# Performance work log

Measured on AMD Instinct MI355X. Metric: run time of the kernel, lower is better.

## Reference

```python
import jax, jax.numpy as jnp
import numpy as np

B, S, D, H, DK, F, K = 8, 1024, 512, 8, 64, 2048, 31
EPS = 1e-5


def _ln(x, g, b):
    m = jnp.mean(x, -1, keepdims=True)
    v = jnp.mean((x - m) ** 2, -1, keepdims=True)
    return (x - m) * jax.lax.rsqrt(v + EPS) * g + b


def _ff(x, w1, b1, w2, b2):
    return jnp.maximum(x @ w1 + b1, 0.0) @ w2 + b2


def setup_inputs() -> dict:
    key = jax.random.key(0)
    ks = jax.random.split(key, 16)
    w = lambda k, shape: jax.random.normal(k, shape, dtype=jnp.float32) * 0.02
    inp = {"x": jax.random.normal(ks[0], (B, S, D), dtype=jnp.float32)}
    for name in ["norm1", "norm2", "norm3", "norm4", "conv_ln"]:
        inp[name + "_g"] = jnp.ones((D,), jnp.float32)
        inp[name + "_b"] = jnp.zeros((D,), jnp.float32)
    # feed-forward 1 and 2
    inp["ff1_w1"] = w(ks[1], (D, F)); inp["ff1_b1"] = jnp.zeros((F,), jnp.float32)
    inp["ff1_w2"] = w(ks[2], (F, D)); inp["ff1_b2"] = jnp.zeros((D,), jnp.float32)
    inp["ff2_w1"] = w(ks[3], (D, F)); inp["ff2_b1"] = jnp.zeros((F,), jnp.float32)
    inp["ff2_w2"] = w(ks[4], (F, D)); inp["ff2_b2"] = jnp.zeros((D,), jnp.float32)
    # attention projections ([in, out] layout)
    inp["wq"] = w(ks[5], (D, D)); inp["bq"] = jnp.zeros((D,), jnp.float32)
    inp["wk"] = w(ks[6], (D, D)); inp["bk"] = jnp.zeros((D,), jnp.float32)
    inp["wv"] = w(ks[7], (D, D)); inp["bv"] = jnp.zeros((D,), jnp.float32)
    inp["wo"] = w(ks[8], (D, D)); inp["bo"] = jnp.zeros((D,), jnp.float32)
    # convolution module
    inp["pw1_w"] = w(ks[9], (D, 2 * D)); inp["pw1_b"] = jnp.zeros((2 * D,), jnp.float32)
    inp["dw_w"] = w(ks[10], (D, 1, K)); inp["dw_b"] = jnp.zeros((D,), jnp.float32)
    inp["bn_g"] = jnp.ones((D,), jnp.float32); inp["bn_b"] = jnp.zeros((D,), jnp.float32)
    inp["bn_mean"] = jnp.zeros((D,), jnp.float32); inp["bn_var"] = jnp.ones((D,), jnp.float32)
    inp["pw2_w"] = w(ks[11], (D, D)); inp["pw2_b"] = jnp.zeros((D,), jnp.float32)
    return inp


def _forward(x, norm1_g, norm1_b, norm2_g, norm2_b, norm3_g, norm3_b, norm4_g, norm4_b,
             ff1_w1, ff1_b1, ff1_w2, ff1_b2, wq, bq, wk, bk, wv, bv, wo, bo,
             conv_ln_g, conv_ln_b, pw1_w, pw1_b, dw_w, dw_b,
             bn_g, bn_b, bn_mean, bn_var, pw2_w, pw2_b,
             ff2_w1, ff2_b1, ff2_w2, ff2_b2):
    b, s, _ = x.shape
    # half-step FF1
    x = x + 0.5 * _ff(_ln(x, norm1_g, norm1_b), ff1_w1, ff1_b1, ff1_w2, ff1_b2)
    # multi-head self-attention (pre-norm)
    h = _ln(x, norm2_g, norm2_b)
    q = (h @ wq + bq).reshape(b, s, H, DK)
    k = (h @ wk + bk).reshape(b, s, H, DK)
    v = (h @ wv + bv).reshape(b, s, H, DK)
    scores = jnp.einsum("bqhd,bkhd->bhqk", q, k) / jnp.sqrt(jnp.asarray(DK, x.dtype))
    attn = jax.nn.softmax(scores, axis=-1)
    o = jnp.einsum("bhqk,bkhd->bqhd", attn, v).reshape(b, s, D)
    x = x + (o @ wo + bo)
    # convolution module (pre-norm)
    h = _ln(x, norm3_g, norm3_b)
    h = _ln(h, conv_ln_g, conv_ln_b)
    h = h @ pw1_w + pw1_b                                 # [B,S,2D] pointwise conv1
    h = h[..., :D] * jax.nn.sigmoid(h[..., D:])           # GLU over channels
    h = h.transpose(0, 2, 1)                              # [B,D,S]
    h = jax.lax.conv_general_dilated(
        h, dw_w, window_strides=(1,), padding=((K // 2, K // 2),),
        feature_group_count=D, dimension_numbers=("NCH", "OIH", "NCH")) + dw_b[:, None]
    h = (h - bn_mean[:, None]) * jax.lax.rsqrt(bn_var + EPS)[:, None] * bn_g[:, None] + bn_b[:, None]
    h = h * jax.nn.sigmoid(h)                             # SiLU
    h = jnp.einsum("bcl,co->bol", h, pw2_w) + pw2_b[:, None]
    x = x + h.transpose(0, 2, 1)
    # half-step FF2
    x = x + 0.5 * _ff(_ln(x, norm4_g, norm4_b), ff2_w1, ff2_b1, ff2_w2, ff2_b2)
    return x


def reference(x, norm1_g, norm1_b, norm2_g, norm2_b, norm3_g, norm3_b, norm4_g, norm4_b,
              conv_ln_g, conv_ln_b, ff1_w1, ff1_b1, ff1_w2, ff1_b2,
              ff2_w1, ff2_b1, ff2_w2, ff2_b2, wq, bq, wk, bk, wv, bv, wo, bo,
              pw1_w, pw1_b, dw_w, dw_b, bn_g, bn_b, bn_mean, bn_var, pw2_w, pw2_b):
    return _forward(x, norm1_g, norm1_b, norm2_g, norm2_b, norm3_g, norm3_b, norm4_g, norm4_b,
                    ff1_w1, ff1_b1, ff1_w2, ff1_b2, wq, bq, wk, bk, wv, bv, wo, bo,
                    conv_ln_g, conv_ln_b, pw1_w, pw1_b, dw_w, dw_b,
                    bn_g, bn_b, bn_mean, bn_var, pw2_w, pw2_b,
                    ff2_w1, ff2_b1, ff2_w2, ff2_b2)
```

## Files before the change

### kernel.cpp

```cpp
#include <hip/hip_runtime.h>
#include <math.h>

#define TOK    8192
#define DMODEL 512
#define FDIM   2048
#define NH     8
#define DKH    64
#define SEQ    1024
#define BATCH  8
#define KCONV  31
#define LN_EPS 1e-5f

typedef __attribute__((ext_vector_type(8))) short bf16x8;
typedef __attribute__((ext_vector_type(4))) float f32x4;
typedef unsigned short ushort_t;

#define AS1 __attribute__((address_space(1)))
#define AS3 __attribute__((address_space(3)))

__device__ __forceinline__ float sigf(float x) { return 1.0f / (1.0f + __expf(-x)); }

__device__ __forceinline__ unsigned short f2bf(float f) {
  unsigned u = __float_as_uint(f);
  u = u + 0x7fffu + ((u >> 16) & 1u);
  return (unsigned short)(u >> 16);
}
__device__ __forceinline__ unsigned pk2(float a, float b) {
  return (unsigned)f2bf(a) | ((unsigned)f2bf(b) << 16);
}
__device__ __forceinline__ float bf2f(ushort_t u) {
  return __uint_as_float((unsigned)u << 16);
}

__device__ __forceinline__ void xcd_swizzle(int gx, int* bx, int* by) {
  const int nwg = gx * (int)gridDim.y;
  const int cpx = nwg >> 3;
  const int bid = (*by) * gx + (*bx);
  const int wg = (bid & 7) * cpx + (bid >> 3);
  *bx = wg % gx;
  *by = wg / gx;
}

struct WJob { const float* src; ushort_t* dst; int K, N, t0; };
struct WJobs {
  WJob j[10];
  int misc_t0;
  const float* dww; const float* bq; const float* bk; const float* bv;
  float* wTc; float* bcat;
};

__global__ __launch_bounds__(256) void wcast_all(WJobs jobs) {
  __shared__ float tile[32][33];
  const int t = blockIdx.x;
  const int tx = threadIdx.x, ty = threadIdx.y;
  if (t >= jobs.misc_t0) {
    const int idx = (t - jobs.misc_t0) * 256 + ty * 32 + tx;
    if (idx < DMODEL * KCONV) {
      const int d = idx / KCONV, k = idx % KCONV;
      jobs.wTc[k * DMODEL + d] = jobs.dww[idx];
    } else if (idx < DMODEL * KCONV + 3 * DMODEL) {
      const int c = idx - DMODEL * KCONV;
      jobs.bcat[c] = (c < DMODEL) ? jobs.bq[c]
                    : (c < 2 * DMODEL ? jobs.bk[c - DMODEL] : jobs.bv[c - 2 * DMODEL]);
    }
    return;
  }
  int i = 0;
#pragma unroll
  for (int k = 1; k < 10; ++k) if (t >= jobs.j[k].t0) i = k;
  const WJob jb = jobs.j[i];
  const int local = t - jb.t0;
  const int ntx = jb.N >> 5;
  const int bx = (local % ntx) * 32, by = (local / ntx) * 32;
#pragma unroll
  for (int r = 0; r < 32; r += 8)
    tile[ty + r][tx] = jb.src[(size_t)(by + ty + r) * jb.N + bx + tx];
  __syncthreads();
#pragma unroll
  for (int r = 0; r < 32; r += 8)
    jb.dst[(size_t)(bx + ty + r) * jb.K + by + tx] = f2bf(tile[tx][ty + r]);
}

template <bool OBF>
__global__ __launch_bounds__(256) void ln_kernel(const float* __restrict__ in,
                                                 const float* __restrict__ g,
                                                 const float* __restrict__ b,
                                                 void* __restrict__ outp) {
  const int wave = threadIdx.x >> 6, lane = threadIdx.x & 63;
  const size_t row = (size_t)blockIdx.x * 4 + wave;
  const float* p = in + row * DMODEL + lane * 8;
  const float4 v0 = *(const float4*)p;
  const float4 v1 = *(const float4*)(p + 4);
  float s  = v0.x + v0.y + v0.z + v0.w + v1.x + v1.y + v1.z + v1.w;
  float ss = v0.x*v0.x + v0.y*v0.y + v0.z*v0.z + v0.w*v0.w
           + v1.x*v1.x + v1.y*v1.y + v1.z*v1.z + v1.w*v1.w;
#pragma unroll
  for (int m = 1; m < 64; m <<= 1) { s += __shfl_xor(s, m); ss += __shfl_xor(ss, m); }
  const float mean = s * (1.0f / DMODEL);
  const float var  = ss * (1.0f / DMODEL) - mean * mean;
  const float rstd = rsqrtf(var + LN_EPS);
  const float4 g0 = *(const float4*)(g + lane * 8);
  const float4 g1 = *(const float4*)(g + lane * 8 + 4);
  const float4 bb0 = *(const float4*)(b + lane * 8);
  const float4 bb1 = *(const float4*)(b + lane * 8 + 4);
  float o[8];
  o[0] = (v0.x - mean) * rstd * g0.x + bb0.x;
  o[1] = (v0.y - mean) * rstd * g0.y + bb0.y;
  o[2] = (v0.z - mean) * rstd * g0.z + bb0.z;
  o[3] = (v0.w - mean) * rstd * g0.w + bb0.w;
  o[4] = (v1.x - mean) * rstd * g1.x + bb1.x;
  o[5] = (v1.y - mean) * rstd * g1.y + bb1.y;
  o[6] = (v1.z - mean) * rstd * g1.z + bb1.z;
  o[7] = (v1.w - mean) * rstd * g1.w + bb1.w;
  if (OBF) {
    uint4 pkv;
    pkv.x = pk2(o[0], o[1]); pkv.y = pk2(o[2], o[3]);
    pkv.z = pk2(o[4], o[5]); pkv.w = pk2(o[6], o[7]);
    *(uint4*)((ushort_t*)outp + row * DMODEL + lane * 8) = pkv;
  } else {
    float4 a, c;
    a.x = o[0]; a.y = o[1]; a.z = o[2]; a.w = o[3];
    c.x = o[4]; c.y = o[5]; c.z = o[6]; c.w = o[7];
    float* q = (float*)outp + row * DMODEL + lane * 8;
    *(float4*)q = a;
    *(float4*)(q + 4) = c;
  }
}

__global__ __launch_bounds__(256) void ln2_kernel(const float* __restrict__ in,
                                                  const float* __restrict__ g1,
                                                  const float* __restrict__ b1,
                                                  const float* __restrict__ g2,
                                                  const float* __restrict__ b2,
                                                  ushort_t* __restrict__ outp) {
  const int wave = threadIdx.x >> 6, lane = threadIdx.x & 63;
  const size_t row = (size_t)blockIdx.x * 4 + wave;
  const float* p = in + row * DMODEL + lane * 8;
  float v[8];
  {
    const float4 v0 = *(const float4*)p;
    const float4 v1 = *(const float4*)(p + 4);
    v[0]=v0.x; v[1]=v0.y; v[2]=v0.z; v[3]=v0.w;
    v[4]=v1.x; v[5]=v1.y; v[6]=v1.z; v[7]=v1.w;
  }
  float s = 0.f, ss = 0.f;
#pragma unroll
  for (int e = 0; e < 8; ++e) { s += v[e]; ss += v[e]*v[e]; }
#pragma unroll
  for (int m = 1; m < 64; m <<= 1) { s += __shfl_xor(s, m); ss += __shfl_xor(ss, m); }
  float mean = s * (1.0f / DMODEL);
  float rstd = rsqrtf(ss * (1.0f / DMODEL) - mean * mean + LN_EPS);
  const float4 ga = *(const float4*)(g1 + lane * 8);
  const float4 gb = *(const float4*)(g1 + lane * 8 + 4);
  const float4 ba = *(const float4*)(b1 + lane * 8);
  const float4 bb = *(const float4*)(b1 + lane * 8 + 4);
  const float gg1[8] = {ga.x,ga.y,ga.z,ga.w,gb.x,gb.y,gb.z,gb.w};
  const float bb1[8] = {ba.x,ba.y,ba.z,ba.w,bb.x,bb.y,bb.z,bb.w};
#pragma unroll
  for (int e = 0; e < 8; ++e) v[e] = (v[e] - mean) * rstd * gg1[e] + bb1[e];
  s = 0.f; ss = 0.f;
#pragma unroll
  for (int e = 0; e < 8; ++e) { s += v[e]; ss += v[e]*v[e]; }
#pragma unroll
  for (int m = 1; m < 64; m <<= 1) { s += __shfl_xor(s, m); ss += __shfl_xor(ss, m); }
  mean = s * (1.0f / DMODEL);
  rstd = rsqrtf(ss * (1.0f / DMODEL) - mean * mean + LN_EPS);
  const float4 gc = *(const float4*)(g2 + lane * 8);
  const float4 gd = *(const float4*)(g2 + lane * 8 + 4);
  const float4 bc = *(const float4*)(b2 + lane * 8);
  const float4 bd = *(const float4*)(b2 + lane * 8 + 4);
  const float gg2[8] = {gc.x,gc.y,gc.z,gc.w,gd.x,gd.y,gd.z,gd.w};
  const float bb2[8] = {bc.x,bc.y,bc.z,bc.w,bd.x,bd.y,bd.z,bd.w};
  float o[8];
#pragma unroll
  for (int e = 0; e < 8; ++e) o[e] = (v[e] - mean) * rstd * gg2[e] + bb2[e];
  uint4 pkv;
  pkv.x = pk2(o[0], o[1]); pkv.y = pk2(o[2], o[3]);
  pkv.z = pk2(o[4], o[5]); pkv.w = pk2(o[6], o[7]);
  *(uint4*)(outp + row * DMODEL + lane * 8) = pkv;
}

template <int ACT, bool QSC>
__global__ __launch_bounds__(512, 2) void gemm256(const ushort_t* __restrict__ A,
                                                  const ushort_t* __restrict__ Bt,
                                                  const float* __restrict__ bias,
                                                  ushort_t* __restrict__ Cout,
                                                  int N) {
  __shared__ ushort_t lds[65536];
  const int t = threadIdx.x;
  const int l = t & 63;
  const int wid = t >> 6;
  const int wm = wid >> 2, wn = wid & 3;
  int bx = blockIdx.x, by = blockIdx.y;
  xcd_swizzle(gridDim.x, &bx, &by);
  const int m0 = by * 256, n0 = bx * 256;
  const int K = 512;

  f32x4 acc[8][4];
#pragma unroll
  for (int m = 0; m < 8; ++m)
#pragma unroll
    for (int n = 0; n < 4; ++n) acc[m][n] = (f32x4){0.f, 0.f, 0.f, 0.f};

  const int srow = t >> 3;
  const int schunk = (t & 7) ^ ((t >> 3) & 7);

#define STAGE_A(TAU, C_, I_)                                                    \
  __builtin_amdgcn_global_load_lds(                                             \
      (const AS1 unsigned*)(A + (size_t)(m0 + (I_) * 64 + srow) * K +           \
                            (TAU) * 64 + schunk * 8),                           \
      (AS3 unsigned*)(lds + (C_) * 16384 + ((I_) * 512 + t) * 8), 16, 0, 0)
#define STAGE_B(TAU, C_, I_)                                                    \
  __builtin_amdgcn_global_load_lds(                                             \
      (const AS1 unsigned*)(Bt + (size_t)(n0 + (I_) * 64 + srow) * K +          \
                            (TAU) * 64 + schunk * 8),                           \
      (AS3 unsigned*)(lds + 32768 + (C_) * 16384 + ((I_) * 512 + t) * 8), 16, 0, 0)

#pragma unroll
  for (int i = 0; i < 4; ++i) STAGE_B(0, 0, i);
#pragma unroll
  for (int i = 0; i < 4; ++i) STAGE_A(0, 0, i);
#pragma unroll
  for (int i = 0; i < 4; ++i) STAGE_B(1, 1, i);
  STAGE_A(1, 1, 0);
  STAGE_A(1, 1, 2);
  asm volatile("s_waitcnt vmcnt(6)" ::: "memory");
  __builtin_amdgcn_s_barrier();

  const int arow = (l & 15);
  const int kch0 = (l >> 4);
  bf16x8 bfr[2][4];

  for (int it = 0; it < 4; ++it) {
    const bool stg = (it < 3);
#pragma unroll
    for (int h = 0; h < 2; ++h) {
      const int c = h;
#pragma unroll
      for (int p = 0; p < 4; ++p) {
        bf16x8 afr[2][2];
#pragma unroll
        for (int m2 = 0; m2 < 2; ++m2)
#pragma unroll
          for (int ks = 0; ks < 2; ++ks) {
            const int row = wm * 128 + (2 * p + m2) * 16 + arow;
            const int ch = (ks * 4 + kch0) ^ (row & 7);
            afr[m2][ks] = *(const bf16x8*)(lds + c * 16384 + row * 64 + ch * 8);
          }
        if (p == 0) {
#pragma unroll
          for (int nr = 0; nr < 4; ++nr)
#pragma unroll
            for (int ks = 0; ks < 2; ++ks) {
              const int row = wn * 64 + nr * 16 + arow;
              const int ch = (ks * 4 + kch0) ^ (row & 7);
              bfr[ks][nr] = *(const bf16x8*)(lds + 32768 + c * 16384 + row * 64 + ch * 8);
            }
        }
        if (p == 0) {
          if (h == 0 || stg) {
            STAGE_A(2 * it + h + 1, c ^ 1, 1);
            STAGE_A(2 * it + h + 1, c ^ 1, 3);
          }
        } else if (p == 1) {
          if (stg) {
#pragma unroll
            for (int i = 0; i < 4; ++i) STAGE_B(2 * it + h + 2, c, i);
          }
        } else if (p == 2) {
          if (stg) {
            STAGE_A(2 * it + h + 2, c, 0);
            STAGE_A(2 * it + h + 2, c, 2);
          }
        }
        __builtin_amdgcn_s_barrier();
        __builtin_amdgcn_s_setprio(1);
#pragma unroll
        for (int ks = 0; ks < 2; ++ks)
#pragma unroll
          for (int m2 = 0; m2 < 2; ++m2)
#pragma unroll
            for (int nr = 0; nr < 4; ++nr)
              acc[2 * p + m2][nr] = __builtin_amdgcn_mfma_f32_16x16x32_bf16(
                  afr[m2][ks], bfr[ks][nr], acc[2 * p + m2][nr], 0, 0, 0);
        __builtin_amdgcn_s_setprio(0);
        if (p == 3) {
          if (h == 0) {
            if (stg) asm volatile("s_waitcnt vmcnt(6)" ::: "memory");
            else     asm volatile("s_waitcnt vmcnt(0)" ::: "memory");
          } else if (stg) {
            asm volatile("s_waitcnt vmcnt(6)" ::: "memory");
          }
        }
        __builtin_amdgcn_s_barrier();
      }
    }
  }
#undef STAGE_A
#undef STAGE_B

#pragma unroll
  for (int m = 0; m < 8; ++m) {
    const int row_b = m0 + wm * 128 + m * 16 + (l >> 4) * 4;
#pragma unroll
    for (int n = 0; n < 4; ++n) {
      const int col = n0 + wn * 64 + n * 16 + (l & 15);
      const float bv = bias[col];
      const float sc = QSC ? (col < DMODEL ? 0.125f : 1.0f) : 1.0f;
#pragma unroll
      for (int j = 0; j < 4; ++j) {
        float v = acc[m][n][j] + bv;
        if (ACT == 1) v = fmaxf(v, 0.f);
        v *= sc;
        Cout[(size_t)(row_b + j) * N + col] = f2bf(v);
      }
    }
  }
}

template <int TN, int ACT, bool RES, bool OBF, bool QSC>
__global__ __launch_bounds__(256) void gemm_bf16(const ushort_t* __restrict__ A,
                                                 const ushort_t* __restrict__ Bt,
                                                 const float* __restrict__ bias,
                                                 const float* __restrict__ Rp,
                                                 float alpha,
                                                 void* __restrict__ Cout,
                                                 int M, int N, int K) {
  constexpr int NF = TN / 32;
  constexpr int NB = TN / 32;
  __shared__ ushort_t Al[128 * 64];
  __shared__ ushort_t Bl[TN * 64];
  const int t = threadIdx.x;
  const int lane = t & 63;
  const int wid = t >> 6;
  const int wr = wid >> 1, wc = wid & 1;
  int bx = blockIdx.x, by = blockIdx.y;
  xcd_swizzle(gridDim.x, &bx, &by);
  const int m0 = by * 128, n0 = bx * TN;

  f32x4 acc[4][NF];
#pragma unroll
  for (int m = 0; m < 4; ++m)
#pragma unroll
    for (int n = 0; n < NF; ++n) acc[m][n] = (f32x4){0.f, 0.f, 0.f, 0.f};

  const int srow = t >> 3;
  const int scol = (t & 7) * 8;
  const ushort_t* Ag = A + (size_t)(m0 + srow) * K + scol;
  const ushort_t* Bg = Bt + (size_t)(n0 + srow) * K + scol;

  for (int k0 = 0; k0 < K; k0 += 64) {
    __syncthreads();
#pragma unroll
    for (int i = 0; i < 4; ++i) {
      __builtin_amdgcn_global_load_lds(
          (const AS1 unsigned*)(Ag + (size_t)i * 32 * K + k0),
          (AS3 unsigned*)(Al + ((size_t)i * 256 + t) * 8),
          16, 0, 0);
    }
#pragma unroll
    for (int i = 0; i < NB; ++i) {
      __builtin_amdgcn_global_load_lds(
          (const AS1 unsigned*)(Bg + (size_t)i * 32 * K + k0),
          (AS3 unsigned*)(Bl + ((size_t)i * 256 + t) * 8),
          16, 0, 0);
    }
    __syncthreads();

#pragma unroll
    for (int ks = 0; ks < 2; ++ks) {
      const int kk = ks * 32 + (lane >> 4) * 8;
      bf16x8 af[4], bfv[NF];
#pragma unroll
      for (int m = 0; m < 4; ++m)
        af[m] = *(const bf16x8*)(Al + (wr * 64 + m * 16 + (lane & 15)) * 64 + kk);
#pragma unroll
      for (int n = 0; n < NF; ++n)
        bfv[n] = *(const bf16x8*)(Bl + (wc * (TN / 2) + n * 16 + (lane & 15)) * 64 + kk);
#pragma unroll
      for (int m = 0; m < 4; ++m)
#pragma unroll
        for (int n = 0; n < NF; ++n)
          acc[m][n] = __builtin_amdgcn_mfma_f32_16x16x32_bf16(af[m], bfv[n], acc[m][n], 0, 0, 0);
    }
  }

#pragma unroll
  for (int m = 0; m < 4; ++m) {
    const int row_b = m0 + wr * 64 + m * 16 + (lane >> 4) * 4;
#pragma unroll
    for (int n = 0; n < NF; ++n) {
      const int col = n0 + wc * (TN / 2) + n * 16 + (lane & 15);
      const float bv = bias[col];
#pragma unroll
      for (int j = 0; j < 4; ++j) {
        float v = acc[m][n][j] + bv;
        if (ACT == 1) v = fmaxf(v, 0.f);
        if (QSC) v *= (col < DMODEL ? 0.125f : 1.0f);
        const size_t idx = (size_t)(row_b + j) * N + col;
        if (RES) v = Rp[idx] + alpha * v;
        if (OBF) ((ushort_t*)Cout)[idx] = f2bf(v);
        else     ((float*)Cout)[idx] = v;
      }
    }
  }
}

__global__ __launch_bounds__(256) void gemm_glu(const ushort_t* __restrict__ A,
                                                const ushort_t* __restrict__ Bt,
                                                const float* __restrict__ bias,
                                                ushort_t* __restrict__ Cout) {
  __shared__ ushort_t Al[128 * 64];
  __shared__ ushort_t Bl[128 * 64];
  const int t = threadIdx.x;
  const int lane = t & 63;
  const int wid = t >> 6;
  const int wr = wid >> 1, wc = wid & 1;
  int bx = blockIdx.x, by = blockIdx.y;
  xcd_swizzle(gridDim.x, &bx, &by);
  const int m0 = by * 128, n0 = bx * 64;
  const int K = DMODEL, N = DMODEL;

  f32x4 aa[4][2], ag[4][2];
#pragma unroll
  for (int m = 0; m < 4; ++m)
#pragma unroll
    for (int n = 0; n < 2; ++n) {
      aa[m][n] = (f32x4){0.f, 0.f, 0.f, 0.f};
      ag[m][n] = (f32x4){0.f, 0.f, 0.f, 0.f};
    }

  const int srow = t >> 3;
  const int scol = (t & 7) * 8;
  const ushort_t* Ag_ = A + (size_t)(m0 + srow) * K + scol;
  const ushort_t* Ba_ = Bt + (size_t)(n0 + srow) * K + scol;
  const ushort_t* Bg_ = Bt + (size_t)(512 + n0 + srow) * K + scol;

  for (int k0 = 0; k0 < K; k0 += 64) {
    __syncthreads();
#pragma unroll
    for (int i = 0; i < 4; ++i) {
      __builtin_amdgcn_global_load_lds(
          (const AS1 unsigned*)(Ag_ + (size_t)i * 32 * K + k0),
          (AS3 unsigned*)(Al + ((size_t)i * 256 + t) * 8),
          16, 0, 0);
    }
#pragma unroll
    for (int i = 0; i < 2; ++i) {
      __builtin_amdgcn_global_load_lds(
          (const AS1 unsigned*)(Ba_ + (size_t)i * 32 * K + k0),
          (AS3 unsigned*)(Bl + ((size_t)i * 256 + t) * 8),
          16, 0, 0);
      __builtin_amdgcn_global_load_lds(
          (const AS1 unsigned*)(Bg_ + (size_t)i * 32 * K + k0),
          (AS3 unsigned*)(Bl + 64 * 64 + ((size_t)i * 256 + t) * 8),
          16, 0, 0);
    }
    __syncthreads();

#pragma unroll
    for (int ks = 0; ks < 2; ++ks) {
      const int kk = ks * 32 + (lane >> 4) * 8;
      bf16x8 af[4], bfa[2], bfg[2];
#pragma unroll
      for (int m = 0; m < 4; ++m)
        af[m] = *(const bf16x8*)(Al + (wr * 64 + m * 16 + (lane & 15)) * 64 + kk);
#pragma unroll
      for (int n = 0; n < 2; ++n) {
        bfa[n] = *(const bf16x8*)(Bl + (wc * 32 + n * 16 + (lane & 15)) * 64 + kk);
        bfg[n] = *(const bf16x8*)(Bl + (64 + wc * 32 + n * 16 + (lane & 15)) * 64 + kk);
      }
#pragma unroll
      for (int m = 0; m < 4; ++m)
#pragma unroll
        for (int n = 0; n < 2; ++n) {
          aa[m][n] = __builtin_amdgcn_mfma_f32_16x16x32_bf16(af[m], bfa[n], aa[m][n], 0, 0, 0);
          ag[m][n] = __builtin_amdgcn_mfma_f32_16x16x32_bf16(af[m], bfg[n], ag[m][n], 0, 0, 0);
        }
    }
  }

#pragma unroll
  for (int m = 0; m < 4; ++m) {
    const int row_b = m0 + wr * 64 + m * 16 + (lane >> 4) * 4;
#pragma unroll
    for (int n = 0; n < 2; ++n) {
      const int col = n0 + wc * 32 + n * 16 + (lane & 15);
      const float ba_v = bias[col];
      const float bg_v = bias[col + DMODEL];
#pragma unroll
      for (int j = 0; j < 4; ++j) {
        const float av = aa[m][n][j] + ba_v;
        const float gv = ag[m][n][j] + bg_v;
        Cout[(size_t)(row_b + j) * N + col] = f2bf(av * sigf(gv));
      }
    }
  }
}

__global__ __launch_bounds__(256) void vtrans(const ushort_t* __restrict__ QKV,
                                              ushort_t* __restrict__ Vt) {
  __shared__ ushort_t tl[64][72];
  const int st = blockIdx.x;
  const int bh = blockIdx.y;
  const int b = bh >> 3, h = bh & 7;
  const int t = threadIdx.x;
#pragma unroll
  for (int i = 0; i < 2; ++i) {
    const int chunk = i * 256 + t;
    const int sr = chunk >> 3, c8 = (chunk & 7) * 8;
    *(uint4*)&tl[sr][c8] =
        *(const uint4*)(QKV + ((size_t)(b * SEQ + st * 64 + sr) * (3 * DMODEL)) + 2 * DMODEL + h * DKH + c8);
  }
  __syncthreads();
#pragma unroll
  for (int i = 0; i < 2; ++i) {
    const int chunk = i * 256 + t;
    const int dr = chunk >> 3, c8 = (chunk & 7) * 8;
    ushort_t tmp[8];
#pragma unroll
    for (int e = 0; e < 8; ++e) tmp[e] = tl[c8 + e][dr];
    *(uint4*)(Vt + ((size_t)(bh * DKH + dr) * SEQ) + st * 64 + c8) = *(uint4*)tmp;
  }
}

__global__ __launch_bounds__(256) void attn_mfma(const ushort_t* __restrict__ QKV,
                                                 const ushort_t* __restrict__ Vt,
                                                 ushort_t* __restrict__ Om) {
  __shared__ ushort_t Ks[128 * 64];
  __shared__ ushort_t Vs[64 * 128];
  __shared__ ushort_t Ps[64 * 128];
  const int t = threadIdx.x;
  const int l = t & 63;
  const int w = t >> 6;
  const int qb = blockIdx.x, h = blockIdx.y, b = blockIdx.z;
  const size_t rowstr = 3 * DMODEL;
  const size_t baseQ = ((size_t)b * SEQ) * rowstr + (size_t)h * DKH;
  const size_t baseK = baseQ + DMODEL;
  const size_t baseV = (size_t)(b * NH + h) * DKH * SEQ;
  const size_t baseO = ((size_t)b * SEQ) * DMODEL + (size_t)h * DKH;

  bf16x8 qf[2];
  {
    const int qrow = qb * 64 + w * 16 + (l & 15);
    const ushort_t* qp = QKV + baseQ + (size_t)qrow * rowstr + ((l >> 4) * 8);
    qf[0] = *(const bf16x8*)(qp);
    qf[1] = *(const bf16x8*)(qp + 32);
  }

  const int krr = t >> 3, kch = t & 7;
  const int vrr = t >> 4, vch = t & 15;

  float mrun[4], lrun[4];
  f32x4 o[4];
#pragma unroll
  for (int j = 0; j < 4; ++j) { mrun[j] = -1e30f; lrun[j] = 0.f; }
#pragma unroll
  for (int n = 0; n < 4; ++n) o[n] = (f32x4){0.f, 0.f, 0.f, 0.f};

  for (int kt = 0; kt < SEQ / 128; ++kt) {
    __syncthreads();
#pragma unroll
    for (int i = 0; i < 4; ++i) {
      const int r = i * 32 + krr;
      __builtin_amdgcn_global_load_lds(
          (const AS1 unsigned*)
              (QKV + baseK + (size_t)(kt * 128 + r) * rowstr + ((kch ^ (r & 7)) * 8)),
          (AS3 unsigned*)(Ks + ((size_t)i * 256 + t) * 8),
          16, 0, 0);
    }
#pragma unroll
    for (int i = 0; i < 4; ++i) {
      const int r = i * 16 + vrr;
      __builtin_amdgcn_global_load_lds(
          (const AS1 unsigned*)
              (Vt + baseV + (size_t)r * SEQ + kt * 128 + ((vch ^ (r & 15)) * 8)),
          (AS3 unsigned*)(Vs + ((size_t)i * 256 + t) * 8),
          16, 0, 0);
    }
    __syncthreads();

    f32x4 s[8];
#pragma unroll
    for (int n = 0; n < 8; ++n) s[n] = (f32x4){0.f, 0.f, 0.f, 0.f};
    __builtin_amdgcn_s_setprio(1);
#pragma unroll
    for (int ks = 0; ks < 2; ++ks) {
      const int kk = ks * 64 + (l >> 4) * 16;
#pragma unroll
      for (int n = 0; n < 8; ++n) {
        const int krow = n * 16 + (l & 15);
        const bf16x8 kf = *(const bf16x8*)((char*)Ks + krow * 128 + (kk ^ ((krow & 7) << 4)));
        s[n] = __builtin_amdgcn_mfma_f32_16x16x32_bf16(qf[ks], kf, s[n], 0, 0, 0);
      }
    }
    __builtin_amdgcn_s_setprio(0);

#pragma unroll
    for (int j = 0; j < 4; ++j) {
      float r0 = s[0][j];
#pragma unroll
      for (int n = 1; n < 8; ++n) r0 = fmaxf(r0, s[n][j]);
      r0 = fmaxf(r0, __shfl_xor(r0, 1));
      r0 = fmaxf(r0, __shfl_xor(r0, 2));
      r0 = fmaxf(r0, __shfl_xor(r0, 4));
      r0 = fmaxf(r0, __shfl_xor(r0, 8));
      const float mn = fmaxf(mrun[j], r0);
      const float cs = __expf(mrun[j] - mn);
      const int prow = w * 16 + (l >> 4) * 4 + j;
      const int pswz = (prow & 15) << 4;
      float psum = 0.f;
#pragma unroll
      for (int n = 0; n < 8; ++n) {
        const float p = __expf(s[n][j] - mn);
        psum += p;
        const int col2 = (n * 16 + (l & 15)) * 2;
        *(ushort_t*)((char*)Ps + prow * 256 + (col2 ^ pswz)) = f2bf(p);
      }
      psum += __shfl_xor(psum, 1);
      psum += __shfl_xor(psum, 2);
      psum += __shfl_xor(psum, 4);
      psum += __shfl_xor(psum, 8);
      lrun[j] = lrun[j] * cs + psum;
      mrun[j] = mn;
      o[0][j] *= cs; o[1][j] *= cs; o[2][j] *= cs; o[3][j] *= cs;
    }

    __builtin_amdgcn_s_setprio(1);
#pragma unroll
    for (int ks = 0; ks < 4; ++ks) {
      const int kk = ks * 64 + (l >> 4) * 16;
      const int arow = w * 16 + (l & 15);
      const bf16x8 pf = *(const bf16x8*)((char*)Ps + arow * 256 + (kk ^ ((arow & 15) << 4)));
#pragma unroll
      for (int n = 0; n < 4; ++n) {
        const int vrow = n * 16 + (l & 15);
        const bf16x8 vf = *(const bf16x8*)((char*)Vs + vrow * 256 + (kk ^ ((vrow & 15) << 4)));
        o[n] = __builtin_amdgcn_mfma_f32_16x16x32_bf16(pf, vf, o[n], 0, 0, 0);
      }
    }
    __builtin_amdgcn_s_setprio(0);
  }

  float inv[4];
#pragma unroll
  for (int j = 0; j < 4; ++j) inv[j] = 1.0f / lrun[j];
#pragma unroll
  for (int j = 0; j < 4; ++j) {
    const int prow = w * 16 + (l >> 4) * 4 + j;
    const int pswz = (prow & 15) << 4;
#pragma unroll
    for (int n = 0; n < 4; ++n) {
      const int col2 = (n * 16 + (l & 15)) * 2;
      *(ushort_t*)((char*)Ps + prow * 256 + (col2 ^ pswz)) = f2bf(o[n][j] * inv[j]);
    }
  }
  __syncthreads();
#pragma unroll
  for (int i = 0; i < 2; ++i) {
    const int chunk = i * 256 + t;
    const int qr = chunk >> 3, c8 = (chunk & 7) * 8;
    const uint4 ov = *(const uint4*)((char*)Ps + qr * 256 + ((c8 * 2) ^ ((qr & 15) << 4)));
    *(uint4*)(Om + baseO + (size_t)(qb * 64 + qr) * DMODEL + c8) = ov;
  }
}

__global__ __launch_bounds__(256) void dwconv_bn_silu(const ushort_t* __restrict__ in,
                                                      const float* __restrict__ wT,
                                                      const float* __restrict__ dwb,
                                                      const float* __restrict__ bng,
                                                      const float* __restrict__ bnb,
                                                      const float* __restrict__ bnm,
                                                      const float* __restrict__ bnv,
                                                      ushort_t* __restrict__ out) {
  const size_t gid = (size_t)blockIdx.x * 256 + threadIdx.x;
  const int dc = (int)(gid & 127) * 4;
  const int s = (int)((gid >> 7) & (SEQ - 1));
  const int b = (int)(gid >> 17);
  const ushort_t* bp = in + (size_t)b * SEQ * DMODEL;
  float ax = 0.f, ay = 0.f, az = 0.f, aw = 0.f;
#pragma unroll
  for (int k = 0; k < KCONV; ++k) {
    const int ssi = s + k - (KCONV / 2);
    if (ssi < 0 || ssi >= SEQ) continue;
    ushort_t xv[4];
    *(uint2*)xv = *(const uint2*)(bp + (size_t)ssi * DMODEL + dc);
    const float4 w = *(const float4*)(wT + k * DMODEL + dc);
    ax = fmaf(bf2f(xv[0]), w.x, ax); ay = fmaf(bf2f(xv[1]), w.y, ay);
    az = fmaf(bf2f(xv[2]), w.z, az); aw = fmaf(bf2f(xv[3]), w.w, aw);
  }
  const float4 bi = *(const float4*)(dwb + dc);
  const float4 mm = *(const float4*)(bnm + dc);
  const float4 vv = *(const float4*)(bnv + dc);
  const float4 gg = *(const float4*)(bng + dc);
  const float4 b2 = *(const float4*)(bnb + dc);
  float v0 = ax + bi.x, v1 = ay + bi.y, v2 = az + bi.z, v3 = aw + bi.w;
  v0 = (v0 - mm.x) * rsqrtf(vv.x + LN_EPS) * gg.x + b2.x;
  v1 = (v1 - mm.y) * rsqrtf(vv.y + LN_EPS) * gg.y + b2.y;
  v2 = (v2 - mm.z) * rsqrtf(vv.z + LN_EPS) * gg.z + b2.z;
  v3 = (v3 - mm.w) * rsqrtf(vv.w + LN_EPS) * gg.w + b2.w;
  v0 = v0 * sigf(v0); v1 = v1 * sigf(v1); v2 = v2 * sigf(v2); v3 = v3 * sigf(v3);
  uint2 o;
  o.x = pk2(v0, v1); o.y = pk2(v2, v3);
  *(uint2*)&out[(((size_t)b * SEQ + s) * DMODEL) + dc] = o;
}

extern "C" void kernel_launch(void* const* d_in, const int* in_sizes, int n_in,
                              void* d_out, int out_size, void* d_ws, size_t ws_size,
                              hipStream_t stream) {
  const float* x    = (const float*)d_in[0];
  const float* n1g  = (const float*)d_in[1];
  const float* n1b  = (const float*)d_in[2];
  const float* n2g  = (const float*)d_in[3];
  const float* n2b  = (const float*)d_in[4];
  const float* n3g  = (const float*)d_in[5];
  const float* n3b  = (const float*)d_in[6];
  const float* n4g  = (const float*)d_in[7];
  const float* n4b  = (const float*)d_in[8];
  const float* clg  = (const float*)d_in[9];
  const float* clb  = (const float*)d_in[10];
  const float* f1w1 = (const float*)d_in[11];
  const float* f1b1 = (const float*)d_in[12];
  const float* f1w2 = (const float*)d_in[13];
  const float* f1b2 = (const float*)d_in[14];
  const float* f2w1 = (const float*)d_in[15];
  const float* f2b1 = (const float*)d_in[16];
  const float* f2w2 = (const float*)d_in[17];
  const float* f2b2 = (const float*)d_in[18];
  const float* wq   = (const float*)d_in[19];
  const float* bq   = (const float*)d_in[20];
  const float* wk   = (const float*)d_in[21];
  const float* bk   = (const float*)d_in[22];
  const float* wv   = (const float*)d_in[23];
  const float* bv   = (const float*)d_in[24];
  const float* wo   = (const float*)d_in[25];
  const float* bo   = (const float*)d_in[26];
  const float* pw1w = (const float*)d_in[27];
  const float* pw1b = (const float*)d_in[28];
  const float* dww  = (const float*)d_in[29];
  const float* dwb  = (const float*)d_in[30];
  const float* bng  = (const float*)d_in[31];
  const float* bnb  = (const float*)d_in[32];
  const float* bnm  = (const float*)d_in[33];
  const float* bnv  = (const float*)d_in[34];
  const float* pw2w = (const float*)d_in[35];
  const float* pw2b = (const float*)d_in[36];

  char* wsb = (char*)d_ws;
  const size_t MB = 1ull << 20;
  ushort_t* Wbf    = (ushort_t*)(wsb + 0);
  ushort_t* f1w1T  = Wbf + 0;
  ushort_t* f1w2T  = Wbf + (1ull << 20);
  ushort_t* f2w1T  = Wbf + (2ull << 20);
  ushort_t* f2w2T  = Wbf + (3ull << 20);
  ushort_t* wqkvT  = Wbf + (4ull << 20);
  ushort_t* wkT    = wqkvT + (256ull << 10);
  ushort_t* wvT    = wqkvT + (512ull << 10);
  ushort_t* woT    = wqkvT + (768ull << 10);
  ushort_t* pw1T   = Wbf + (5ull << 20);
  ushort_t* pw2T   = Wbf + (5ull << 20) + (512ull << 10);
  float*    WTc    = (float*)(wsb + 12 * MB);
  float*    bcat   = (float*)(wsb + 12 * MB + 128 * 1024);
  ushort_t* Lbf    = (ushort_t*)(wsb + 13 * MB);
  ushort_t* Hbf    = (ushort_t*)(wsb + 21 * MB);
  ushort_t* QKVb   = (ushort_t*)(wsb + 53 * MB);
  ushort_t* Vtb    = (ushort_t*)(wsb + 77 * MB);
  ushort_t* Gbf    = (ushort_t*)(wsb + 53 * MB);
  ushort_t* Obf    = (ushort_t*)(wsb + 85 * MB);
  ushort_t* Cbf    = Obf;
  float* out = (float*)d_out;

  const dim3 blk(256);
  const dim3 blk512(512);
  const dim3 blkT(32, 8);
  const dim3 gLN(TOK / 4);
  const dim3 gFFa256(FDIM / 256, TOK / 256);
  const dim3 gQKV256(3 * DMODEL / 256, TOK / 256);
  const dim3 gFFb(DMODEL / 64, TOK / 128);
  const dim3 gGLU(DMODEL / 64, TOK / 128);
  const dim3 gAttn(SEQ / 64, NH, BATCH);
  const dim3 gVt(SEQ / 64, BATCH * NH);
  const dim3 gElem(TOK * 128 / 256);

  {
    WJobs jobs;
    const float* srcs[10] = {f1w1, f1w2, f2w1, f2w2, wq, wk, wv, wo, pw1w, pw2w};
    ushort_t* dsts[10] = {f1w1T, f1w2T, f2w1T, f2w2T, wqkvT, wkT, wvT, woT, pw1T, pw2T};
    const int Ks[10] = {512, 2048, 512, 2048, 512, 512, 512, 512, 512, 512};
    const int Ns[10] = {2048, 512, 2048, 512, 512, 512, 512, 512, 1024, 512};
    int t0 = 0;
    for (int i = 0; i < 10; ++i) {
      jobs.j[i].src = srcs[i]; jobs.j[i].dst = dsts[i];
      jobs.j[i].K = Ks[i]; jobs.j[i].N = Ns[i]; jobs.j[i].t0 = t0;
      t0 += (Ks[i] / 32) * (Ns[i] / 32);
    }
    jobs.misc_t0 = t0;
    jobs.dww = dww; jobs.bq = bq; jobs.bk = bk; jobs.bv = bv;
    jobs.wTc = WTc; jobs.bcat = bcat;
    const int nmisc = (DMODEL * KCONV + 3 * DMODEL + 255) / 256;
    wcast_all<<<t0 + nmisc, blkT, 0, stream>>>(jobs);
  }

  ln_kernel<true><<<gLN, blk, 0, stream>>>(x, n1g, n1b, Lbf);
  gemm256<1, false><<<gFFa256, blk512, 0, stream>>>(Lbf, f1w1T, f1b1, Hbf, FDIM);
  gemm_bf16<64,  0, true,  false, false><<<gFFb, blk, 0, stream>>>(Hbf, f1w2T, f1b2, x, 0.5f, out, TOK, DMODEL, FDIM);

  ln_kernel<true><<<gLN, blk, 0, stream>>>(out, n2g, n2b, Lbf);
  gemm256<0, true><<<gQKV256, blk512, 0, stream>>>(Lbf, wqkvT, bcat, QKVb, 3 * DMODEL);
  vtrans<<<gVt, blk, 0, stream>>>(QKVb, Vtb);
  attn_mfma<<<gAttn, blk, 0, stream>>>(QKVb, Vtb, Obf);
  gemm_bf16<64,  0, true,  false, false><<<gFFb, blk, 0, stream>>>(Obf, woT, bo, out, 1.0f, out, TOK, DMODEL, DMODEL);

  ln2_kernel<<<gLN, blk, 0, stream>>>(out, n3g, n3b, clg, clb, Lbf);
  gemm_glu<<<gGLU, blk, 0, stream>>>(Lbf, pw1T, pw1b, Gbf);
  dwconv_bn_silu<<<gElem, blk, 0, stream>>>(Gbf, WTc, dwb, bng, bnb, bnm, bnv, Cbf);
  gemm_bf16<64,  0, true,  false, false><<<gFFb, blk, 0, stream>>>(Cbf, pw2T, pw2b, out, 1.0f, out, TOK, DMODEL, DMODEL);

  ln_kernel<true><<<gLN, blk, 0, stream>>>(out, n4g, n4b, Lbf);
  gemm256<1, false><<<gFFa256, blk512, 0, stream>>>(Lbf, f2w1T, f2b1, Hbf, FDIM);
  gemm_bf16<64,  0, true,  false, false><<<gFFb, blk, 0, stream>>>(Hbf, f2w2T, f2b2, out, 0.5f, out, TOK, DMODEL, FDIM);
}
```

Baseline: 312.4 us.

## Fold log2e into Q scale, use exp2 in softmax, widen dwconv to 8 channels

The Q projection scale becomes 0.125*log2(e), so attention softmax can use exp2f in place of __expf, which saves a multiply per exponential. The row-max reduction is rewritten as a balanced tree to shorten the dependency chain. The depthwise conv kernel now has each thread handle 8 channels with 16-byte loads and stores, halving the thread count and widening memory accesses, at the cost of more registers per thread.

```diff
diff --git a/kernel.cpp b/kernel.cpp
--- a/kernel.cpp
+++ b/kernel.cpp
@@ -17,6 +17,8 @@
 
 #define AS1 __attribute__((address_space(1)))
 #define AS3 __attribute__((address_space(3)))
+
+#define QSCALE 0.1803368801111204f
 
 __device__ __forceinline__ float sigf(float x) { return 1.0f / (1.0f + __expf(-x)); }
 
@@ -306,7 +308,7 @@
     for (int n = 0; n < 4; ++n) {
       const int col = n0 + wn * 64 + n * 16 + (l & 15);
       const float bv = bias[col];
-      const float sc = QSC ? (col < DMODEL ? 0.125f : 1.0f) : 1.0f;
+      const float sc = QSC ? (col < DMODEL ? QSCALE : 1.0f) : 1.0f;
 #pragma unroll
       for (int j = 0; j < 4; ++j) {
         float v = acc[m][n][j] + bv;
@@ -396,7 +398,7 @@
       for (int j = 0; j < 4; ++j) {
         float v = acc[m][n][j] + bv;
         if (ACT == 1) v = fmaxf(v, 0.f);
-        if (QSC) v *= (col < DMODEL ? 0.125f : 1.0f);
+        if (QSC) v *= (col < DMODEL ? QSCALE : 1.0f);
         const size_t idx = (size_t)(row_b + j) * N + col;
         if (RES) v = Rp[idx] + alpha * v;
         if (OBF) ((ushort_t*)Cout)[idx] = f2bf(v);
@@ -598,21 +600,20 @@
 
 #pragma unroll
     for (int j = 0; j < 4; ++j) {
-      float r0 = s[0][j];
-#pragma unroll
-      for (int n = 1; n < 8; ++n) r0 = fmaxf(r0, s[n][j]);
+      float r0 = fmaxf(fmaxf(fmaxf(s[0][j], s[1][j]), fmaxf(s[2][j], s[3][j])),
+                       fmaxf(fmaxf(s[4][j], s[5][j]), fmaxf(s[6][j], s[7][j])));
       r0 = fmaxf(r0, __shfl_xor(r0, 1));
       r0 = fmaxf(r0, __shfl_xor(r0, 2));
       r0 = fmaxf(r0, __shfl_xor(r0, 4));
       r0 = fmaxf(r0, __shfl_xor(r0, 8));
       const float mn = fmaxf(mrun[j], r0);
-      const float cs = __expf(mrun[j] - mn);
+      const float cs = exp2f(mrun[j] - mn);
       const int prow = w * 16 + (l >> 4) * 4 + j;
       const int pswz = (prow & 15) << 4;
       float psum = 0.f;
 #pragma unroll
       for (int n = 0; n < 8; ++n) {
-        const float p = __expf(s[n][j] - mn);
+        const float p = exp2f(s[n][j] - mn);
         psum += p;
         const int col2 = (n * 16 + (l & 15)) * 2;
         *(ushort_t*)((char*)Ps + prow * 256 + (col2 ^ pswz)) = f2bf(p);
@@ -674,35 +675,51 @@
                                                       const float* __restrict__ bnv,
                                                       ushort_t* __restrict__ out) {
   const size_t gid = (size_t)blockIdx.x * 256 + threadIdx.x;
-  const int dc = (int)(gid & 127) * 4;
-  const int s = (int)((gid >> 7) & (SEQ - 1));
-  const int b = (int)(gid >> 17);
+  const int dc = (int)(gid & 63) * 8;
+  const int s = (int)((gid >> 6) & (SEQ - 1));
+  const int b = (int)(gid >> 16);
   const ushort_t* bp = in + (size_t)b * SEQ * DMODEL;
-  float ax = 0.f, ay = 0.f, az = 0.f, aw = 0.f;
+  float a[8];
+#pragma unroll
+  for (int e = 0; e < 8; ++e) a[e] = 0.f;
 #pragma unroll
   for (int k = 0; k < KCONV; ++k) {
     const int ssi = s + k - (KCONV / 2);
     if (ssi < 0 || ssi >= SEQ) continue;
-    ushort_t xv[4];
-    *(uint2*)xv = *(const uint2*)(bp + (size_t)ssi * DMODEL + dc);
-    const float4 w = *(const float4*)(wT + k * DMODEL + dc);
-    ax = fmaf(bf2f(xv[0]), w.x, ax); ay = fmaf(bf2f(xv[1]), w.y, ay);
-    az = fmaf(bf2f(xv[2]), w.z, az); aw = fmaf(bf2f(xv[3]), w.w, aw);
-  }
-  const float4 bi = *(const float4*)(dwb + dc);
-  const float4 mm = *(const float4*)(bnm + dc);
-  const float4 vv = *(const float4*)(bnv + dc);
-  const float4 gg = *(const float4*)(bng + dc);
-  const float4 b2 = *(const float4*)(bnb + dc);
-  float v0 = ax + bi.x, v1 = ay + bi.y, v2 = az + bi.z, v3 = aw + bi.w;
-  v0 = (v0 - mm.x) * rsqrtf(vv.x + LN_EPS) * gg.x + b2.x;
-  v1 = (v1 - mm.y) * rsqrtf(vv.y + LN_EPS) * gg.y + b2.y;
-  v2 = (v2 - mm.z) * rsqrtf(vv.z + LN_EPS) * gg.z + b2.z;
-  v3 = (v3 - mm.w) * rsqrtf(vv.w + LN_EPS) * gg.w + b2.w;
-  v0 = v0 * sigf(v0); v1 = v1 * sigf(v1); v2 = v2 * sigf(v2); v3 = v3 * sigf(v3);
-  uint2 o;
-  o.x = pk2(v0, v1); o.y = pk2(v2, v3);
-  *(uint2*)&out[(((size_t)b * SEQ + s) * DMODEL) + dc] = o;
+    ushort_t xv[8];
+    *(uint4*)xv = *(const uint4*)(bp + (size_t)ssi * DMODEL + dc);
+    const float4 w0 = *(const float4*)(wT + k * DMODEL + dc);
+    const float4 w1 = *(const float4*)(wT + k * DMODEL + dc + 4);
+    a[0] = fmaf(bf2f(xv[0]), w0.x, a[0]); a[1] = fmaf(bf2f(xv[1]), w0.y, a[1]);
+    a[2] = fmaf(bf2f(xv[2]), w0.z, a[2]); a[3] = fmaf(bf2f(xv[3]), w0.w, a[3]);
+    a[4] = fmaf(bf2f(xv[4]), w1.x, a[4]); a[5] = fmaf(bf2f(xv[5]), w1.y, a[5]);
+    a[6] = fmaf(bf2f(xv[6]), w1.z, a[6]); a[7] = fmaf(bf2f(xv[7]), w1.w, a[7]);
+  }
+  float v[8];
+#pragma unroll
+  for (int half = 0; half < 2; ++half) {
+    const int d4 = dc + half * 4;
+    const float4 bi = *(const float4*)(dwb + d4);
+    const float4 mm = *(const float4*)(bnm + d4);
+    const float4 vv = *(const float4*)(bnv + d4);
+    const float4 gg = *(const float4*)(bng + d4);
+    const float4 b2 = *(const float4*)(bnb + d4);
+    const float bia[4] = {bi.x, bi.y, bi.z, bi.w};
+    const float mma[4] = {mm.x, mm.y, mm.z, mm.w};
+    const float vva[4] = {vv.x, vv.y, vv.z, vv.w};
+    const float gga[4] = {gg.x, gg.y, gg.z, gg.w};
+    const float b2a[4] = {b2.x, b2.y, b2.z, b2.w};
+#pragma unroll
+    for (int e = 0; e < 4; ++e) {
+      float t0 = a[half * 4 + e] + bia[e];
+      t0 = (t0 - mma[e]) * rsqrtf(vva[e] + LN_EPS) * gga[e] + b2a[e];
+      v[half * 4 + e] = t0 * sigf(t0);
+    }
+  }
+  uint4 o;
+  o.x = pk2(v[0], v[1]); o.y = pk2(v[2], v[3]);
+  o.z = pk2(v[4], v[5]); o.w = pk2(v[6], v[7]);
+  *(uint4*)&out[(((size_t)b * SEQ + s) * DMODEL) + dc] = o;
 }
 
 extern "C" void kernel_launch(void* const* d_in, const int* in_sizes, int n_in,
@@ -780,7 +797,7 @@
   const dim3 gGLU(DMODEL / 64, TOK / 128);
   const dim3 gAttn(SEQ / 64, NH, BATCH);
   const dim3 gVt(SEQ / 64, BATCH * NH);
-  const dim3 gElem(TOK * 128 / 256);
+  const dim3 gConv(TOK * 64 / 256);
 
   {
     WJobs jobs;
@@ -813,7 +830,7 @@
 
   ln2_kernel<<<gLN, blk, 0, stream>>>(out, n3g, n3b, clg, clb, Lbf);
   gemm_glu<<<gGLU, blk, 0, stream>>>(Lbf, pw1T, pw1b, Gbf);
-  dwconv_bn_silu<<<gElem, blk, 0, stream>>>(Gbf, WTc, dwb, bng, bnb, bnm, bnv, Cbf);
+  dwconv_bn_silu<<<gConv, blk, 0, stream>>>(Gbf, WTc, dwb, bng, bnb, bnm, bnv, Cbf);
   gemm_bf16<64,  0, true,  false, false><<<gFFb, blk, 0, stream>>>(Cbf, pw2T, pw2b, out, 1.0f, out, TOK, DMODEL, DMODEL);
 
   ln_kernel<true><<<gLN, blk, 0, stream>>>(out, n4g, n4b, Lbf);
```

Measured after the change: 311.0 us. Within noise of the previous version (-0.4%).
